# Optimization experiments

Measured on AMD Instinct MI355X. Metric: run time of the kernel, lower is better.

## Reference

```python
import jax, jax.numpy as jnp
import numpy as np

D = 16
EPS = 1e-15


def setup_inputs() -> dict:
    key = jax.random.key(0)
    k1, k2 = jax.random.split(key)
    B, C, H, W = 8, 384, 64, 64  # C = heads(8) * 3 * D(16)
    K = 512
    qkv = jax.random.normal(k1, (B, C, H, W), dtype=jnp.float32)
    codebook = jax.random.normal(k2, (K, D), dtype=jnp.float32)
    return {"qkv": qkv, "codebook": codebook}


def reference(qkv, codebook):
    B, C, H, W = qkv.shape
    K = codebook.shape[0]
    # (B, heads, 3D, HW) -> (B, heads, HW, 3D)
    x = qkv.reshape(B, -1, 3 * D, H * W).transpose(0, 1, 3, 2)
    q = x[..., 0:D].reshape(-1, D)          # (N, D)
    k = x[..., D:2 * D].reshape(-1, D)      # (N, D)
    v = x[..., 2 * D:].reshape(-1, D)       # (N, D)
    # vector quantization: nearest codebook entry by squared L2
    # ||k - c||^2 = ||k||^2 - 2 k.c + ||c||^2 ; ||k||^2 constant over argmin
    dist = jnp.sum(codebook * codebook, axis=-1)[None, :] - 2.0 * (k @ codebook.T)
    indices = jnp.argmin(dist, axis=-1)     # (N,) int, detached (non-diff)
    # O_tV = one_hot.T @ v  -> per-code sum of v
    O_tV = jax.ops.segment_sum(v, indices, num_segments=K)          # (K, D)
    # counts = one_hot.T @ ones  (denominator collapses to exp(QC_t) @ counts)
    counts = jax.ops.segment_sum(jnp.ones_like(indices, dtype=q.dtype), indices, num_segments=K)  # (K,)
    QC_t = q @ codebook.T                   # (N, K)
    E = jnp.exp(QC_t)                       # (N, K)
    numerator = E @ O_tV                    # (N, D)
    denominator = E @ counts + EPS          # (N,)
    result = numerator / denominator[:, None]
    return result.reshape(B, -1, H, W)      # (B, heads*D, H, W)
```

## Files before the change

### kernel.cpp

```cpp
#include <hip/hip_runtime.h>

typedef short short8 __attribute__((ext_vector_type(8)));
typedef float floatx4 __attribute__((ext_vector_type(4)));

#define D16 16
#define KC 512
#define NTOK (8 * 8 * 4096)


__device__ __forceinline__ unsigned short rne_bf16(float x) {
    unsigned u = __float_as_uint(x);
    return (unsigned short)((u + 0x7fffu + ((u >> 16) & 1u)) >> 16);
}
__device__ __forceinline__ float bf16_to_f32(unsigned short h) {
    return __uint_as_float(((unsigned)h) << 16);
}

extern "C" __global__ __launch_bounds__(256)
void vq_assign(const float* __restrict__ qkv, const float* __restrict__ cb,
               unsigned short* __restrict__ idx)
{
    __shared__ alignas(16) unsigned short s_cbh[KC * 16];
    __shared__ alignas(16) unsigned short s_cbr[KC * 16];
    __shared__ float s_cn[KC];
    __shared__ float s_kf[4][16][17];
    int tid = threadIdx.x;
    for (int i = tid; i < KC * 16; i += 256) {
        float x = cb[i];
        unsigned short h = rne_bf16(x);
        s_cbh[i] = h;
        s_cbr[i] = rne_bf16(x - bf16_to_f32(h));
    }
    for (int j = tid; j < KC; j += 256) {
        float s = 0.f;
#pragma unroll
        for (int d = 0; d < D16; ++d) { float c = cb[j * D16 + d]; s = fmaf(c, c, s); }
        s_cn[j] = s;
    }
    __syncthreads();

    int lane = tid & 63;
    int col = lane & 15;
    int half8 = ((lane >> 4) & 1) * 8;
    bool hiHalf = lane < 32;
    int wv = tid >> 6;
    int tile0 = (blockIdx.x * 4 + wv) * 4;

    for (int t = 0; t < 4; ++t) {
        int tok0 = (tile0 + t) * 16;
        int bh = tok0 >> 12;
        const float* kbase = qkv + (size_t)bh * (48 * 4096) + 16 * 4096 + (tok0 & 4095);

        short8 a8;
        {
            const float* p = kbase + (size_t)half8 * 4096 + col;
#pragma unroll
            for (int i = 0; i < 8; ++i) {
                float x = p[(size_t)i * 4096];
                unsigned short h = rne_bf16(x);
                a8[i] = hiHalf ? (short)h : (short)rne_bf16(x - bf16_to_f32(h));
                if (hiHalf) s_kf[wv][col][half8 + i] = x;
            }
        }
        __builtin_amdgcn_wave_barrier();

        float p1[4], p2[4];
#pragma unroll
        for (int r = 0; r < 4; ++r) { p1[r] = -3.4e38f; p2[r] = -3.4e38f; }

        for (int c = 0; c < 32; ++c) {
            int code = c * 16 + col;
            short8 b1 = *(const short8*)(&s_cbh[code * 16 + half8]);
            short8 b2 = (short8)0;
            if (hiHalf) b2 = *(const short8*)(&s_cbr[code * 16 + half8]);
            float cn2 = -0.5f * s_cn[code];
            floatx4 acc = { cn2, cn2, cn2, cn2 };
            acc = __builtin_amdgcn_mfma_f32_16x16x32_bf16(a8, b1, acc, 0, 0, 0);
            acc = __builtin_amdgcn_mfma_f32_16x16x32_bf16(a8, b2, acc, 0, 0, 0);
#pragma unroll
            for (int r = 0; r < 4; ++r) {
                unsigned sb = (__float_as_uint(acc[r]) & 0xFFFFFE00u) | (unsigned)code;
                float sp = __uint_as_float(sb);
                float old1 = p1[r];
                p1[r] = fmaxf(old1, sp);
                p2[r] = fmaxf(p2[r], fminf(old1, sp));
            }
        }
#pragma unroll
        for (int m = 1; m < 16; m <<= 1) {
#pragma unroll
            for (int r = 0; r < 4; ++r) {
                float o1 = __shfl_xor(p1[r], m, 64);
                float o2 = __shfl_xor(p2[r], m, 64);
                float n1 = fmaxf(p1[r], o1);
                float n2 = fmaxf(fminf(p1[r], o1), fmaxf(p2[r], o2));
                p1[r] = n1; p2[r] = n2;
            }
        }
        if (col < 4) {
            int c1 = 0, c2 = 0;
#pragma unroll
            for (int r = 0; r < 4; ++r) {
                if (col == r) {
                    c1 = (int)(__float_as_uint(p1[r]) & 511u);
                    c2 = (int)(__float_as_uint(p2[r]) & 511u);
                }
            }
            int tokrow = (lane >> 4) * 4 + col;
            const float* kf = &s_kf[wv][tokrow][0];
            const float* cb1 = cb + c1 * D16;
            const float* cb2 = cb + c2 * D16;
            float dot1 = 0.f, dot2 = 0.f;
#pragma unroll
            for (int d = 0; d < D16; ++d) {
                float kx = kf[d];
                dot1 = fmaf(kx, cb1[d], dot1);
                dot2 = fmaf(kx, cb2[d], dot2);
            }
            float d1 = fmaf(-2.f, dot1, s_cn[c1]);
            float d2 = fmaf(-2.f, dot2, s_cn[c2]);
            int jw = (d2 < d1 || (d2 == d1 && c2 < c1)) ? c2 : c1;
            idx[tok0 + tokrow] = (unsigned short)jw;
        }
        __builtin_amdgcn_wave_barrier();
    }
}

extern "C" __global__ __launch_bounds__(256)
void vq_segsum(const float* __restrict__ qkv, const unsigned short* __restrict__ idx,
               float* __restrict__ M)
{
    __shared__ float s_acc[KC * 17];
    for (int i = threadIdx.x; i < KC * 17; i += 256) s_acc[i] = 0.f;
    __syncthreads();

    for (int n = blockIdx.x * 256 + threadIdx.x; n < NTOK; n += gridDim.x * 256) {
        int bh = n >> 12, hw = n & 4095;
        const float* bv = qkv + (size_t)bh * (48 * 4096) + hw + 32 * 4096;
        int bj = idx[n];
#pragma unroll
        for (int d = 0; d < D16; ++d)
            atomicAdd(&s_acc[bj * 17 + d], bv[d * 4096]);
        atomicAdd(&s_acc[bj * 17 + 16], 1.0f);
    }
    __syncthreads();
    for (int i = threadIdx.x; i < KC * 17; i += 256)
        atomicAdd(&M[i], s_acc[i]);
}

extern "C" __global__ __launch_bounds__(256)
void vq_attend(const float* __restrict__ qkv, const float* __restrict__ cb,
               const float* __restrict__ M, float* __restrict__ out)
{
    __shared__ alignas(16) unsigned short s_cbh[KC * 16];
    __shared__ alignas(16) unsigned short s_mt[16 * 520];
    __shared__ float s_cnt[KC];
    __shared__ alignas(16) unsigned short s_w[4][2][16 * 40];

    int tid = threadIdx.x;
    for (int i = tid; i < KC * 16; i += 256) s_cbh[i] = rne_bf16(cb[i]);
    for (int i = tid; i < KC * 17; i += 256) {
        int j = i / 17, d = i - j * 17;
        float x = M[i];
        if (d == 16) s_cnt[j] = x;
        else s_mt[d * 520 + j] = rne_bf16(x);
    }
    __syncthreads();

    int lane = tid & 63;
    int col = lane & 15;
    int g = lane >> 4;
    int half8 = (g & 1) * 8;
    bool hiHalf = lane < 32;
    int wv_id = tid >> 6;
    unsigned short* wtA = &s_w[wv_id][0][0];
    unsigned short* wtB = &s_w[wv_id][1][0];
    int tile0 = (blockIdx.x * 4 + wv_id) * 4;

    int wr_row = g * 4;
    int wsel0 = (((col >> 3) + 0) ^ g) * 8 + (col & 7);
    int wsel1 = (((col >> 3) + 2) ^ g) * 8 + (col & 7);
    int w_rd = col * 40 + ((g ^ (col >> 2)) << 3);

    for (int tp = 0; tp < 2; ++tp) {
        int tokA = (tile0 + 2 * tp) * 16;
        int tokB = tokA + 16;

        short8 aA, aB;
        {
            const float* p = qkv + (size_t)(tokA >> 12) * (48 * 4096) + (tokA & 4095)
                           + (size_t)half8 * 4096 + col;
#pragma unroll
            for (int i = 0; i < 8; ++i) {
                float x = p[(size_t)i * 4096];
                unsigned short h = rne_bf16(x);
                aA[i] = hiHalf ? (short)h : (short)rne_bf16(x - bf16_to_f32(h));
            }
        }
        {
            const float* p = qkv + (size_t)(tokB >> 12) * (48 * 4096) + (tokB & 4095)
                           + (size_t)half8 * 4096 + col;
#pragma unroll
            for (int i = 0; i < 8; ++i) {
                float x = p[(size_t)i * 4096];
                unsigned short h = rne_bf16(x);
                aB[i] = hiHalf ? (short)h : (short)rne_bf16(x - bf16_to_f32(h));
            }
        }

        floatx4 oA = {0.f, 0.f, 0.f, 0.f}, oB = {0.f, 0.f, 0.f, 0.f};
        float denA[4] = {0.f, 0.f, 0.f, 0.f}, denB[4] = {0.f, 0.f, 0.f, 0.f};

        for (int c32 = 0; c32 < 16; ++c32) {
#pragma unroll
            for (int cg = 0; cg < 2; ++cg) {
                int code = (c32 * 2 + cg) * 16 + col;
                short8 b1 = *(const short8*)(&s_cbh[code * 16 + half8]);
                floatx4 sA = {0.f, 0.f, 0.f, 0.f}, sB = {0.f, 0.f, 0.f, 0.f};
                sA = __builtin_amdgcn_mfma_f32_16x16x32_bf16(aA, b1, sA, 0, 0, 0);
                sB = __builtin_amdgcn_mfma_f32_16x16x32_bf16(aB, b1, sB, 0, 0, 0);
                float cnt = s_cnt[code];
                int wsel = cg ? wsel1 : wsel0;
#pragma unroll
                for (int r = 0; r < 4; ++r) {
                    int base = (wr_row + r) * 40 + wsel;
                    float wA = __expf(sA[r]);
                    unsigned uA = __float_as_uint(wA) & 0xffff0000u;
                    denA[r] = fmaf(__uint_as_float(uA), cnt, denA[r]);
                    wtA[base] = (unsigned short)(uA >> 16);
                    float wB = __expf(sB[r]);
                    unsigned uB = __float_as_uint(wB) & 0xffff0000u;
                    denB[r] = fmaf(__uint_as_float(uB), cnt, denB[r]);
                    wtB[base] = (unsigned short)(uB >> 16);
                }
            }
            short8 mb  = *(const short8*)(&s_mt[col * 520 + c32 * 32 + g * 8]);
            short8 wfA = *(const short8*)(&wtA[w_rd]);
            short8 wfB = *(const short8*)(&wtB[w_rd]);
            oA = __builtin_amdgcn_mfma_f32_16x16x32_bf16(wfA, mb, oA, 0, 0, 0);
            oB = __builtin_amdgcn_mfma_f32_16x16x32_bf16(wfB, mb, oB, 0, 0, 0);
        }
#pragma unroll
        for (int m = 1; m < 16; m <<= 1) {
#pragma unroll
            for (int r = 0; r < 4; ++r) {
                denA[r] += __shfl_xor(denA[r], m, 64);
                denB[r] += __shfl_xor(denB[r], m, 64);
            }
        }
#pragma unroll
        for (int r = 0; r < 4; ++r) {
            int row = g * 4 + r;
            out[(size_t)(tokA + row) * D16 + col] = oA[r] / (denA[r] + 1e-15f);
            out[(size_t)(tokB + row) * D16 + col] = oB[r] / (denB[r] + 1e-15f);
        }
    }
}

extern "C" void kernel_launch(void* const* d_in, const int* in_sizes, int n_in,
                              void* d_out, int out_size, void* d_ws, size_t ws_size,
                              hipStream_t stream) {
    const float* qkv = (const float*)d_in[0];
    const float* cb  = (const float*)d_in[1];
    float* out = (float*)d_out;

    float* M = (float*)d_ws;
    unsigned short* idx = (unsigned short*)((char*)d_ws + 36864);

    hipMemsetAsync(d_ws, 0, KC * 17 * sizeof(float), stream);

    vq_assign<<<NTOK / 256, 256, 0, stream>>>(qkv, cb, idx);
    vq_segsum<<<1024, 256, 0, stream>>>(qkv, idx, M);
    vq_attend<<<NTOK / 256, 256, 0, stream>>>(qkv, cb, M, out);
}
```

Before: 255.3 us.

## Transpose attend MFMA so exp weights stay in registers, drop LDS staging

The attend kernel now computes the score tile transposed (codebook as the A operand, q as B), with the codebook split into hi/lo bf16 and permuted in shared memory. The exp weights then land directly in the register layout needed for the second MFMA and are packed with a perm instruction, which removes the per-wave LDS write/read round trip and the wide denominator shuffle reduction. Segsum gets one launch per 512 tokens with a fixed two-token unroll, and it skips flushing empty codes to global memory. The new code adds codebook permutation logic that must exactly match the MFMA layouts, and the hi/lo split now sits on the codebook instead of q, which changes rounding slightly.

```diff
diff --git a/kernel.cpp b/kernel.cpp
--- a/kernel.cpp
+++ b/kernel.cpp
@@ -14,6 +14,9 @@
 }
 __device__ __forceinline__ float bf16_to_f32(unsigned short h) {
     return __uint_as_float(((unsigned)h) << 16);
+}
+__device__ __forceinline__ unsigned pk_hi16(unsigned uy, unsigned ux) {
+    return __builtin_amdgcn_perm(uy, ux, 0x07060302u);
 }
 
 extern "C" __global__ __launch_bounds__(256)
@@ -134,31 +137,48 @@
     for (int i = threadIdx.x; i < KC * 17; i += 256) s_acc[i] = 0.f;
     __syncthreads();
 
-    for (int n = blockIdx.x * 256 + threadIdx.x; n < NTOK; n += gridDim.x * 256) {
+#pragma unroll
+    for (int u = 0; u < 2; ++u) {
+        int n = blockIdx.x * 512 + u * 256 + threadIdx.x;
         int bh = n >> 12, hw = n & 4095;
         const float* bv = qkv + (size_t)bh * (48 * 4096) + hw + 32 * 4096;
         int bj = idx[n];
 #pragma unroll
         for (int d = 0; d < D16; ++d)
-            atomicAdd(&s_acc[bj * 17 + d], bv[d * 4096]);
+            atomicAdd(&s_acc[bj * 17 + d], bv[(size_t)d * 4096]);
         atomicAdd(&s_acc[bj * 17 + 16], 1.0f);
     }
     __syncthreads();
-    for (int i = threadIdx.x; i < KC * 17; i += 256)
-        atomicAdd(&M[i], s_acc[i]);
+    for (int j = threadIdx.x; j < KC; j += 256) {
+        float c = s_acc[j * 17 + 16];
+        if (c != 0.f) {
+#pragma unroll
+            for (int d = 0; d < D16; ++d)
+                atomicAdd(&M[j * 17 + d], s_acc[j * 17 + d]);
+            atomicAdd(&M[j * 17 + 16], c);
+        }
+    }
 }
 
 extern "C" __global__ __launch_bounds__(256)
 void vq_attend(const float* __restrict__ qkv, const float* __restrict__ cb,
                const float* __restrict__ M, float* __restrict__ out)
 {
-    __shared__ alignas(16) unsigned short s_cbh[KC * 16];
+    __shared__ alignas(16) unsigned short s_cb2[KC * 40];
     __shared__ alignas(16) unsigned short s_mt[16 * 520];
-    __shared__ float s_cnt[KC];
-    __shared__ alignas(16) unsigned short s_w[4][2][16 * 40];
+    __shared__ alignas(16) float s_cnt[KC];
 
     int tid = threadIdx.x;
-    for (int i = tid; i < KC * 16; i += 256) s_cbh[i] = rne_bf16(cb[i]);
+    for (int e = tid; e < KC * 16; e += 256) {
+        int rho = e >> 4, d = e & 15;
+        int b = rho >> 5, w = rho & 31;
+        int h = w >> 4, m = w & 15;
+        int j = b * 32 + (m >> 2) * 8 + h * 4 + (m & 3);
+        float x = cb[j * 16 + d];
+        unsigned short hh = rne_bf16(x);
+        s_cb2[rho * 40 + d] = hh;
+        s_cb2[rho * 40 + 16 + d] = rne_bf16(x - bf16_to_f32(hh));
+    }
     for (int i = tid; i < KC * 17; i += 256) {
         int j = i / 17, d = i - j * 17;
         float x = M[i];
@@ -170,89 +190,101 @@
     int lane = tid & 63;
     int col = lane & 15;
     int g = lane >> 4;
-    int half8 = (g & 1) * 8;
-    bool hiHalf = lane < 32;
     int wv_id = tid >> 6;
-    unsigned short* wtA = &s_w[wv_id][0][0];
-    unsigned short* wtB = &s_w[wv_id][1][0];
     int tile0 = (blockIdx.x * 4 + wv_id) * 4;
-
-    int wr_row = g * 4;
-    int wsel0 = (((col >> 3) + 0) ^ g) * 8 + (col & 7);
-    int wsel1 = (((col >> 3) + 2) ^ g) * 8 + (col & 7);
-    int w_rd = col * 40 + ((g ^ (col >> 2)) << 3);
 
     for (int tp = 0; tp < 2; ++tp) {
         int tokA = (tile0 + 2 * tp) * 16;
         int tokB = tokA + 16;
 
-        short8 aA, aB;
+        short8 qA, qB;
         {
             const float* p = qkv + (size_t)(tokA >> 12) * (48 * 4096) + (tokA & 4095)
-                           + (size_t)half8 * 4096 + col;
-#pragma unroll
-            for (int i = 0; i < 8; ++i) {
-                float x = p[(size_t)i * 4096];
-                unsigned short h = rne_bf16(x);
-                aA[i] = hiHalf ? (short)h : (short)rne_bf16(x - bf16_to_f32(h));
-            }
+                           + (size_t)((g & 1) * 8) * 4096 + col;
+#pragma unroll
+            for (int i = 0; i < 8; ++i) qA[i] = (short)rne_bf16(p[(size_t)i * 4096]);
         }
         {
             const float* p = qkv + (size_t)(tokB >> 12) * (48 * 4096) + (tokB & 4095)
-                           + (size_t)half8 * 4096 + col;
-#pragma unroll
-            for (int i = 0; i < 8; ++i) {
-                float x = p[(size_t)i * 4096];
-                unsigned short h = rne_bf16(x);
-                aB[i] = hiHalf ? (short)h : (short)rne_bf16(x - bf16_to_f32(h));
-            }
+                           + (size_t)((g & 1) * 8) * 4096 + col;
+#pragma unroll
+            for (int i = 0; i < 8; ++i) qB[i] = (short)rne_bf16(p[(size_t)i * 4096]);
         }
 
         floatx4 oA = {0.f, 0.f, 0.f, 0.f}, oB = {0.f, 0.f, 0.f, 0.f};
-        float denA[4] = {0.f, 0.f, 0.f, 0.f}, denB[4] = {0.f, 0.f, 0.f, 0.f};
-
-        for (int c32 = 0; c32 < 16; ++c32) {
-#pragma unroll
-            for (int cg = 0; cg < 2; ++cg) {
-                int code = (c32 * 2 + cg) * 16 + col;
-                short8 b1 = *(const short8*)(&s_cbh[code * 16 + half8]);
-                floatx4 sA = {0.f, 0.f, 0.f, 0.f}, sB = {0.f, 0.f, 0.f, 0.f};
-                sA = __builtin_amdgcn_mfma_f32_16x16x32_bf16(aA, b1, sA, 0, 0, 0);
-                sB = __builtin_amdgcn_mfma_f32_16x16x32_bf16(aB, b1, sB, 0, 0, 0);
-                float cnt = s_cnt[code];
-                int wsel = cg ? wsel1 : wsel0;
-#pragma unroll
-                for (int r = 0; r < 4; ++r) {
-                    int base = (wr_row + r) * 40 + wsel;
-                    float wA = __expf(sA[r]);
-                    unsigned uA = __float_as_uint(wA) & 0xffff0000u;
-                    denA[r] = fmaf(__uint_as_float(uA), cnt, denA[r]);
-                    wtA[base] = (unsigned short)(uA >> 16);
-                    float wB = __expf(sB[r]);
-                    unsigned uB = __float_as_uint(wB) & 0xffff0000u;
-                    denB[r] = fmaf(__uint_as_float(uB), cnt, denB[r]);
-                    wtB[base] = (unsigned short)(uB >> 16);
-                }
-            }
-            short8 mb  = *(const short8*)(&s_mt[col * 520 + c32 * 32 + g * 8]);
-            short8 wfA = *(const short8*)(&wtA[w_rd]);
-            short8 wfB = *(const short8*)(&wtB[w_rd]);
-            oA = __builtin_amdgcn_mfma_f32_16x16x32_bf16(wfA, mb, oA, 0, 0, 0);
-            oB = __builtin_amdgcn_mfma_f32_16x16x32_bf16(wfB, mb, oB, 0, 0, 0);
-        }
-#pragma unroll
-        for (int m = 1; m < 16; m <<= 1) {
-#pragma unroll
-            for (int r = 0; r < 4; ++r) {
-                denA[r] += __shfl_xor(denA[r], m, 64);
-                denB[r] += __shfl_xor(denB[r], m, 64);
-            }
-        }
+        float denA = 0.f, denB = 0.f;
+
+        for (int b = 0; b < 16; ++b) {
+            short8 A0 = *(const short8*)(&s_cb2[(b * 32 + col) * 40 + g * 8]);
+            short8 A1 = *(const short8*)(&s_cb2[(b * 32 + 16 + col) * 40 + g * 8]);
+            float4 cn0 = *(const float4*)(&s_cnt[b * 32 + g * 8]);
+            float4 cn1 = *(const float4*)(&s_cnt[b * 32 + g * 8 + 4]);
+            floatx4 z = {0.f, 0.f, 0.f, 0.f};
+            floatx4 sA0 = __builtin_amdgcn_mfma_f32_16x16x32_bf16(A0, qA, z, 0, 0, 0);
+            floatx4 sA1 = __builtin_amdgcn_mfma_f32_16x16x32_bf16(A1, qA, z, 0, 0, 0);
+            floatx4 sB0 = __builtin_amdgcn_mfma_f32_16x16x32_bf16(A0, qB, z, 0, 0, 0);
+            floatx4 sB1 = __builtin_amdgcn_mfma_f32_16x16x32_bf16(A1, qB, z, 0, 0, 0);
+            short8 mb = *(const short8*)(&s_mt[col * 520 + b * 32 + g * 8]);
+
+            union { unsigned u[4]; short8 s8; } paA, paB;
+            {
+                unsigned u0 = __float_as_uint(__expf(sA0[0]));
+                unsigned u1 = __float_as_uint(__expf(sA0[1]));
+                unsigned u2 = __float_as_uint(__expf(sA0[2]));
+                unsigned u3 = __float_as_uint(__expf(sA0[3]));
+                unsigned u4 = __float_as_uint(__expf(sA1[0]));
+                unsigned u5 = __float_as_uint(__expf(sA1[1]));
+                unsigned u6 = __float_as_uint(__expf(sA1[2]));
+                unsigned u7 = __float_as_uint(__expf(sA1[3]));
+                denA = fmaf(__uint_as_float(u0 & 0xffff0000u), cn0.x, denA);
+                denA = fmaf(__uint_as_float(u1 & 0xffff0000u), cn0.y, denA);
+                denA = fmaf(__uint_as_float(u2 & 0xffff0000u), cn0.z, denA);
+                denA = fmaf(__uint_as_float(u3 & 0xffff0000u), cn0.w, denA);
+                denA = fmaf(__uint_as_float(u4 & 0xffff0000u), cn1.x, denA);
+                denA = fmaf(__uint_as_float(u5 & 0xffff0000u), cn1.y, denA);
+                denA = fmaf(__uint_as_float(u6 & 0xffff0000u), cn1.z, denA);
+                denA = fmaf(__uint_as_float(u7 & 0xffff0000u), cn1.w, denA);
+                paA.u[0] = pk_hi16(u1, u0);
+                paA.u[1] = pk_hi16(u3, u2);
+                paA.u[2] = pk_hi16(u5, u4);
+                paA.u[3] = pk_hi16(u7, u6);
+            }
+            {
+                unsigned u0 = __float_as_uint(__expf(sB0[0]));
+                unsigned u1 = __float_as_uint(__expf(sB0[1]));
+                unsigned u2 = __float_as_uint(__expf(sB0[2]));
+                unsigned u3 = __float_as_uint(__expf(sB0[3]));
+                unsigned u4 = __float_as_uint(__expf(sB1[0]));
+                unsigned u5 = __float_as_uint(__expf(sB1[1]));
+                unsigned u6 = __float_as_uint(__expf(sB1[2]));
+                unsigned u7 = __float_as_uint(__expf(sB1[3]));
+                denB = fmaf(__uint_as_float(u0 & 0xffff0000u), cn0.x, denB);
+                denB = fmaf(__uint_as_float(u1 & 0xffff0000u), cn0.y, denB);
+                denB = fmaf(__uint_as_float(u2 & 0xffff0000u), cn0.z, denB);
+                denB = fmaf(__uint_as_float(u3 & 0xffff0000u), cn0.w, denB);
+                denB = fmaf(__uint_as_float(u4 & 0xffff0000u), cn1.x, denB);
+                denB = fmaf(__uint_as_float(u5 & 0xffff0000u), cn1.y, denB);
+                denB = fmaf(__uint_as_float(u6 & 0xffff0000u), cn1.z, denB);
+                denB = fmaf(__uint_as_float(u7 & 0xffff0000u), cn1.w, denB);
+                paB.u[0] = pk_hi16(u1, u0);
+                paB.u[1] = pk_hi16(u3, u2);
+                paB.u[2] = pk_hi16(u5, u4);
+                paB.u[3] = pk_hi16(u7, u6);
+            }
+            oA = __builtin_amdgcn_mfma_f32_16x16x32_bf16(paA.s8, mb, oA, 0, 0, 0);
+            oB = __builtin_amdgcn_mfma_f32_16x16x32_bf16(paB.s8, mb, oB, 0, 0, 0);
+        }
+        denA += __shfl_xor(denA, 16, 64);
+        denA += __shfl_xor(denA, 32, 64);
+        denB += __shfl_xor(denB, 16, 64);
+        denB += __shfl_xor(denB, 32, 64);
 #pragma unroll
         for (int r = 0; r < 4; ++r) {
             int row = g * 4 + r;
-            out[(size_t)(tokA + row) * D16 + col] = oA[r] / (denA[r] + 1e-15f);
-            out[(size_t)(tokB + row) * D16 + col] = oB[r] / (denB[r] + 1e-15f);
+            float dA = __shfl(denA, row, 64);
+            float dB = __shfl(denB, row, 64);
+            out[(size_t)(tokA + row) * D16 + col] = oA[r] / (dA + 1e-15f);
+            out[(size_t)(tokB + row) * D16 + col] = oB[r] / (dB + 1e-15f);
         }
     }
 }
@@ -270,6 +302,6 @@
     hipMemsetAsync(d_ws, 0, KC * 17 * sizeof(float), stream);
 
     vq_assign<<<NTOK / 256, 256, 0, stream>>>(qkv, cb, idx);
-    vq_segsum<<<1024, 256, 0, stream>>>(qkv, idx, M);
+    vq_segsum<<<NTOK / 512, 256, 0, stream>>>(qkv, idx, M);
     vq_attend<<<NTOK / 256, 256, 0, stream>>>(qkv, cb, M, out);
 }
```

Result: slower. 461.7 us (+80.8%).
